# Optimization experiments

Hardware: AMD Instinct MI355X
Metric: run time of the kernel (lower is better)

The kernel has to match this reference:

```python
import jax, jax.numpy as jnp
import numpy as np

N, E, D, ED = 10000, 50000, 32, 16
DIMS = [(D, 8 * D), (8 * D, 16 * D), (16 * D, 16 * D), (16 * D, 16 * D)]
BI_OUT = 8 * D + ED  # 272


def _gat(h, src, dst, ea, Wl, Wr, We, att, b, n):
    """GATv2Conv, heads=1: score = att . leaky_relu(Wl x_j + Wr x_i + We e_ij); msg = Wl x_j."""
    xl = h @ Wl
    xr = h @ Wr
    ee = ea @ We
    s = jax.nn.leaky_relu(xl[src] + xr[dst] + ee, 0.2)   # [E_aug, out]
    alpha = s @ att                                       # [E_aug]
    amax = jax.lax.stop_gradient(jax.ops.segment_max(alpha, dst, num_segments=n))
    ex = jnp.exp(alpha - amax[dst])
    den = jax.ops.segment_sum(ex, dst, num_segments=n)
    w = ex / jnp.maximum(den[dst], 1e-16)
    return jax.ops.segment_sum(xl[src] * w[:, None], dst, num_segments=n) + b


def _forward(x, edge_attr, Wl0, Wr0, We0, a0, b0, Wl1, Wr1, We1, a1, b1,
             Wl2, Wr2, We2, a2, b2, Wl3, Wr3, We3, a3, b3,
             Wbi, bbi, Wm1, bm1, Wm2, bm2, Wm3, bm3, edge_index):
    src, dst = edge_index[0], edge_index[1]
    # self loops with edge_attr fill_value='mean' (mean of incoming edge_attr per target node)
    cnt = jax.ops.segment_sum(jnp.ones((E,), jnp.float32), dst, num_segments=N)
    mean_attr = jax.ops.segment_sum(edge_attr, dst, num_segments=N) / jnp.maximum(cnt, 1.0)[:, None]
    loop = jnp.arange(N, dtype=edge_index.dtype)
    src_a = jnp.concatenate([src, loop])
    dst_a = jnp.concatenate([dst, loop])
    ea_a = jnp.concatenate([edge_attr, mean_attr], axis=0)

    h = x
    layers = [(Wl0, Wr0, We0, a0, b0), (Wl1, Wr1, We1, a1, b1),
              (Wl2, Wr2, We2, a2, b2), (Wl3, Wr3, We3, a3, b3)]
    for i, (Wl, Wr, We, a, b) in enumerate(layers):
        h = _gat(h, src_a, dst_a, ea_a, Wl, Wr, We, a, b, N)
        if i < 3:
            h = jax.nn.relu(h)

    # edge scoring: gather both endpoints, bilinear with edge_attr, then MLP -> sigmoid
    z = jnp.concatenate([h[src], h[dst]], axis=1)           # [E, 2*16*D] = [E, 1024]
    bi = jnp.einsum('ni,kij,nj->nk', z, Wbi, edge_attr) + bbi  # [E, 272]
    m = jax.nn.relu(bi @ Wm1 + bm1)
    m = jax.nn.relu(m @ Wm2 + bm2)
    return jax.nn.sigmoid(m @ Wm3 + bm3)                    # [E, 1]


def setup_inputs() -> dict:
    ki = iter(jax.random.split(jax.random.key(0), 40))

    def rn(shape, s=0.05):
        return jax.random.normal(next(ki), shape, dtype=jnp.float32) * s

    inp = {
        "x": rn((N, D), 1.0),
        "edge_attr": rn((E, ED), 1.0),
        "edge_index": jax.random.randint(next(ki), (2, E), 0, N, dtype=jnp.int32),
    }
    for i, (din, dout) in enumerate(DIMS):
        inp[f"Wl{i}"] = rn((din, dout))
        inp[f"Wr{i}"] = rn((din, dout))
        inp[f"We{i}"] = rn((ED, dout))
        inp[f"a{i}"] = rn((dout,))
        inp[f"b{i}"] = jnp.zeros((dout,), jnp.float32)
    inp["Wbi"] = rn((BI_OUT, 2 * 16 * D, ED), 0.02)
    inp["bbi"] = jnp.zeros((BI_OUT,), jnp.float32)
    inp["Wm1"] = rn((BI_OUT, BI_OUT))
    inp["bm1"] = jnp.zeros((BI_OUT,), jnp.float32)
    inp["Wm2"] = rn((BI_OUT, D))
    inp["bm2"] = jnp.zeros((D,), jnp.float32)
    inp["Wm3"] = rn((D, 1))
    inp["bm3"] = jnp.zeros((1,), jnp.float32)
    return inp


def reference(x, edge_attr, edge_index, Wl0, Wr0, We0, a0, b0, Wl1, Wr1, We1, a1, b1,
              Wl2, Wr2, We2, a2, b2, Wl3, Wr3, We3, a3, b3,
              Wbi, bbi, Wm1, bm1, Wm2, bm2, Wm3, bm3):
    return _forward(x, edge_attr, Wl0, Wr0, We0, a0, b0, Wl1, Wr1, We1, a1, b1,
                    Wl2, Wr2, We2, a2, b2, Wl3, Wr3, We3, a3, b3,
                    Wbi, bbi, Wm1, bm1, Wm2, bm2, Wm3, bm3, edge_index)
```

## Files before the change

kernel.cpp:

```cpp
#include <hip/hip_runtime.h>
#include <hip/hip_bf16.h>
#include <hip/hip_fp16.h>
#include <cstdio>

#define N_NODES 10000
#define M_NODEP 10240
#define N_EDGES 50000
#define M_EDGEP 50176
#define E_AUG   60000
#define E_AUGP  60160
#define ED      16
#define BI_OUT  272
#define KP      288

typedef __attribute__((ext_vector_type(8))) short s16x8;
typedef __attribute__((ext_vector_type(4))) short s16x4;
typedef __attribute__((ext_vector_type(8))) _Float16 h16x8;
typedef __attribute__((ext_vector_type(4))) _Float16 h16x4;
typedef __attribute__((ext_vector_type(4))) float f32x4;

__device__ inline void stc(float* p, float v){ *p = v; }
__device__ inline void stc(__hip_bfloat16* p, float v){ *p = __float2bfloat16(v); }
__device__ inline void stc(__half* p, float v){ *p = __float2half(v); }
__device__ inline float bf2f(short s){ return __uint_as_float(((unsigned)(unsigned short)s) << 16); }
__device__ inline short f2bf(float f){ __hip_bfloat16 h = __float2bfloat16(f); return *(short*)&h; }

__device__ __forceinline__ void gl2lds16(const void* g, void* l){
  __builtin_amdgcn_global_load_lds((const __attribute__((address_space(1))) void*)g,
                                   (__attribute__((address_space(3))) void*)l, 16, 0, 0);
}

__device__ inline size_t preidx(int n, int k, int kSteps){
  int nb = n >> 7, f = (n >> 4) & 7, r = n & 15;
  int s = k >> 5, q = (k >> 3) & 3, ii = k & 7;
  return ((((size_t)nb*kSteps + s)*8 + f)*64 + q*16 + r)*8 + ii;
}

__global__ void edge_attr_sum_k(const float* __restrict__ ea, const int* __restrict__ ei,
                                float* __restrict__ meanat, float* __restrict__ cntF){
  int t = blockIdx.x*256 + threadIdx.x;
  if (t >= N_EDGES*ED) return;
  int e = t >> 4, j = t & 15;
  int dst = ei[N_EDGES + e];
  atomicAdd(&meanat[dst*ED + j], ea[t]);
  if (j == 0) atomicAdd(&cntF[dst], 1.0f);
}

__global__ void mean_div_k(float* __restrict__ meanat, const float* __restrict__ cntF){
  int t = blockIdx.x*256 + threadIdx.x;
  if (t >= N_NODES*ED) return;
  meanat[t] /= fmaxf(cntF[t>>4], 1.0f);
}

__global__ void scan_k(const float* __restrict__ cntF, int* __restrict__ rowptr){
  __shared__ int s[1024];
  int tid = threadIdx.x;
  int loc[10]; int sum = 0;
  #pragma unroll
  for (int k = 0; k < 10; ++k){
    int i = tid*10 + k;
    int v = (i < N_NODES) ? ((int)cntF[i] + 1) : 0;
    loc[k] = sum; sum += v;
  }
  s[tid] = sum; __syncthreads();
  for (int off = 1; off < 1024; off <<= 1){
    int t2 = (tid >= off) ? s[tid-off] : 0;
    __syncthreads();
    s[tid] += t2;
    __syncthreads();
  }
  int pre = s[tid] - sum;
  #pragma unroll
  for (int k = 0; k < 10; ++k){
    int i = tid*10 + k;
    if (i < N_NODES) rowptr[i] = pre + loc[k];
  }
  if (tid == 1023) rowptr[N_NODES] = s[1023];
}

__global__ void scatter_k(const int* __restrict__ ei, const int* __restrict__ rowptr,
                          int* __restrict__ fill, int* __restrict__ csr){
  int e = blockIdx.x*256 + threadIdx.x;
  if (e >= E_AUG) return;
  int dst = (e < N_EDGES) ? ei[N_EDGES+e] : (e - N_EDGES);
  int pos = rowptr[dst] + atomicAdd(&fill[dst], 1);
  csr[pos] = e;
}

template<typename TC, bool BIAS, bool RELU>
__global__ __launch_bounds__(256)
void mfma_gemm_k(const __hip_bfloat16* __restrict__ A, const __hip_bfloat16* __restrict__ Bp,
                 TC* __restrict__ C, const float* __restrict__ bias,
                 int Mstore, int K, int lda, int ldc){
  __shared__ __align__(16) __hip_bfloat16 Asm[2][4096];
  const int tid = threadIdx.x;
  const int lane = tid & 63, wave = tid >> 6;
  const int wm = (wave >> 1) * 64, wn = (wave & 1) * 64;
  const int m0 = blockIdx.x * 128, n0 = blockIdx.y * 128;
  const int quad = lane >> 4, r16 = lane & 15;
  const int kSteps = K >> 5;

  f32x4 acc[4][4];
  #pragma unroll
  for (int i = 0; i < 4; ++i)
    #pragma unroll
    for (int j = 0; j < 4; ++j)
      acc[i][j] = (f32x4){0.f, 0.f, 0.f, 0.f};

  const int rl = lane >> 2, cq = lane & 3;
  const int row0 = wave*32 + rl;
  const int qg = (cq - ((row0 >> 1) & 3)) & 3;
  const __hip_bfloat16* ga0 = &A[(size_t)(m0 + row0)*lda + qg*8];
  const __hip_bfloat16* ga1 = &A[(size_t)(m0 + row0 + 16)*lda + qg*8];
  const int aoff0 = (wave*32)*32, aoff1 = (wave*32 + 16)*32;

  const __hip_bfloat16* gB = Bp + (((size_t)blockIdx.y*kSteps)*8 + (wn >> 4))*512 + (size_t)lane*8;

  gl2lds16(ga0, &Asm[0][aoff0]);
  gl2lds16(ga1, &Asm[0][aoff1]);
  s16x8 bcur[4], bnxt[4];
  #pragma unroll
  for (int j = 0; j < 4; ++j) bcur[j] = *(const s16x8*)(gB + j*512);

  for (int s = 0; s < kSteps; ++s){
    __syncthreads();
    if (s + 1 < kSteps){
      int k0 = (s + 1) * 32;
      gl2lds16(ga0 + k0, &Asm[(s+1)&1][aoff0]);
      gl2lds16(ga1 + k0, &Asm[(s+1)&1][aoff1]);
      const __hip_bfloat16* gBn = gB + (size_t)(s+1)*4096;
      #pragma unroll
      for (int j = 0; j < 4; ++j) bnxt[j] = *(const s16x8*)(gBn + j*512);
    }
    s16x8 af[4];
    #pragma unroll
    for (int i = 0; i < 4; ++i){
      int row = wm + i*16 + r16;
      af[i] = *(const s16x8*)&Asm[s & 1][row*32 + (((quad + (row >> 1)) & 3) << 3)];
    }
    #pragma unroll
    for (int i = 0; i < 4; ++i)
      #pragma unroll
      for (int j = 0; j < 4; ++j)
        acc[i][j] = __builtin_amdgcn_mfma_f32_16x16x32_bf16(af[i], bcur[j], acc[i][j], 0, 0, 0);
    #pragma unroll
    for (int j = 0; j < 4; ++j) bcur[j] = bnxt[j];
  }
  #pragma unroll
  for (int i = 0; i < 4; ++i){
    #pragma unroll
    for (int reg = 0; reg < 4; ++reg){
      int gr = m0 + wm + i*16 + quad*4 + reg;
      if (gr >= Mstore) continue;
      #pragma unroll
      for (int j = 0; j < 4; ++j){
        int gc = n0 + wn + j*16 + r16;
        float v = acc[i][j][reg];
        if (BIAS) v += bias[gc];
        if (RELU) v = fmaxf(v, 0.f);
        stc(&C[(size_t)gr*ldc + gc], v);
      }
    }
  }
}

template<typename TC>
__global__ __launch_bounds__(256)
void gemm_k32_k(const __hip_bfloat16* __restrict__ A, const __hip_bfloat16* __restrict__ Bp,
                TC* __restrict__ C, int Mstore, int Ntiles, int lda, int ldc){
  __shared__ __align__(16) __hip_bfloat16 Asm[4096];
  const int tid = threadIdx.x;
  const int lane = tid & 63, wave = tid >> 6;
  const int wm = (wave >> 1) * 64, wn = (wave & 1) * 64;
  const int m0 = blockIdx.x * 128;
  const int quad = lane >> 4, r16 = lane & 15;

  const int rl = lane >> 2, cq = lane & 3;
  const int row0 = wave*32 + rl;
  const int qg = (cq - ((row0 >> 1) & 3)) & 3;
  gl2lds16(&A[(size_t)(m0 + row0)*lda + qg*8],      &Asm[(wave*32)*32]);
  gl2lds16(&A[(size_t)(m0 + row0 + 16)*lda + qg*8], &Asm[(wave*32 + 16)*32]);
  __syncthreads();
  s16x8 af[4];
  #pragma unroll
  for (int i = 0; i < 4; ++i){
    int row = wm + i*16 + r16;
    af[i] = *(const s16x8*)&Asm[row*32 + (((quad + (row >> 1)) & 3) << 3)];
  }

  const __hip_bfloat16* gB = Bp + (size_t)(wn >> 4)*512 + (size_t)lane*8;
  s16x8 bcur[4], bnxt[4];
  #pragma unroll
  for (int j = 0; j < 4; ++j) bcur[j] = *(const s16x8*)(gB + j*512);

  for (int nt = 0; nt < Ntiles; ++nt){
    if (nt + 1 < Ntiles){
      const __hip_bfloat16* gBn = gB + (size_t)(nt+1)*4096;
      #pragma unroll
      for (int j = 0; j < 4; ++j) bnxt[j] = *(const s16x8*)(gBn + j*512);
    }
    f32x4 acc[4][4];
    #pragma unroll
    for (int i = 0; i < 4; ++i)
      #pragma unroll
      for (int j = 0; j < 4; ++j)
        acc[i][j] = (f32x4){0.f, 0.f, 0.f, 0.f};
    #pragma unroll
    for (int i = 0; i < 4; ++i)
      #pragma unroll
      for (int j = 0; j < 4; ++j)
        acc[i][j] = __builtin_amdgcn_mfma_f32_16x16x32_bf16(af[i], bcur[j], acc[i][j], 0, 0, 0);
    int n0 = nt*128;
    #pragma unroll
    for (int i = 0; i < 4; ++i){
      #pragma unroll
      for (int reg = 0; reg < 4; ++reg){
        int gr = m0 + wm + i*16 + quad*4 + reg;
        if (gr >= Mstore) continue;
        #pragma unroll
        for (int j = 0; j < 4; ++j)
          stc(&C[(size_t)gr*ldc + n0 + wn + j*16 + r16], acc[i][j][reg]);
      }
    }
    #pragma unroll
    for (int j = 0; j < 4; ++j) bcur[j] = bnxt[j];
  }
}

__global__ __launch_bounds__(256)
void mlp2_out_k(const __hip_bfloat16* __restrict__ A, const __hip_bfloat16* __restrict__ Bp,
                const float* __restrict__ bias, const float* __restrict__ Wm3,
                const float* __restrict__ bm3, float* __restrict__ out,
                int Mstore, int K, int lda){
  __shared__ __align__(16) __hip_bfloat16 Asm[2][4096];
  const int tid = threadIdx.x;
  const int lane = tid & 63, wave = tid >> 6;
  const int wm = (wave >> 1) * 64, wn = (wave & 1) * 64;
  const int m0 = blockIdx.x * 128;
  const int quad = lane >> 4, r16 = lane & 15;
  const int kSteps = K >> 5;

  f32x4 acc[4][2];
  #pragma unroll
  for (int i = 0; i < 4; ++i)
    #pragma unroll
    for (int j = 0; j < 2; ++j)
      acc[i][j] = (f32x4){0.f, 0.f, 0.f, 0.f};

  const int rl = lane >> 2, cq = lane & 3;
  const int row0 = wave*32 + rl;
  const int qg = (cq - ((row0 >> 1) & 3)) & 3;
  const __hip_bfloat16* ga0 = &A[(size_t)(m0 + row0)*lda + qg*8];
  const __hip_bfloat16* ga1 = &A[(size_t)(m0 + row0 + 16)*lda + qg*8];
  const int aoff0 = (wave*32)*32, aoff1 = (wave*32 + 16)*32;

  const __hip_bfloat16* gB = Bp + (size_t)(wn >> 4)*512 + (size_t)lane*8;

  gl2lds16(ga0, &Asm[0][aoff0]);
  gl2lds16(ga1, &Asm[0][aoff1]);
  s16x8 bcur[2], bnxt[2];
  #pragma unroll
  for (int j = 0; j < 2; ++j) bcur[j] = *(const s16x8*)(gB + j*512);

  for (int s = 0; s < kSteps; ++s){
    __syncthreads();
    if (s + 1 < kSteps){
      int k0 = (s + 1) * 32;
      gl2lds16(ga0 + k0, &Asm[(s+1)&1][aoff0]);
      gl2lds16(ga1 + k0, &Asm[(s+1)&1][aoff1]);
      const __hip_bfloat16* gBn = gB + (size_t)(s+1)*4096;
      #pragma unroll
      for (int j = 0; j < 2; ++j) bnxt[j] = *(const s16x8*)(gBn + j*512);
    }
    s16x8 af[4];
    #pragma unroll
    for (int i = 0; i < 4; ++i){
      int row = wm + i*16 + r16;
      af[i] = *(const s16x8*)&Asm[s & 1][row*32 + (((quad + (row >> 1)) & 3) << 3)];
    }
    #pragma unroll
    for (int i = 0; i < 4; ++i)
      #pragma unroll
      for (int j = 0; j < 2; ++j)
        acc[i][j] = __builtin_amdgcn_mfma_f32_16x16x32_bf16(af[i], bcur[j], acc[i][j], 0, 0, 0);
    #pragma unroll
    for (int j = 0; j < 2; ++j) bcur[j] = bnxt[j];
  }
  if (wn == 0){
    float w3a = Wm3[r16], w3b = Wm3[16 + r16];
    float ba = bias[r16], bb = bias[16 + r16];
    #pragma unroll
    for (int i = 0; i < 4; ++i){
      #pragma unroll
      for (int reg = 0; reg < 4; ++reg){
        int gr = m0 + wm + i*16 + quad*4 + reg;
        float v0 = fmaxf(acc[i][0][reg] + ba, 0.f);
        float v1 = fmaxf(acc[i][1][reg] + bb, 0.f);
        float dot = v0*w3a + v1*w3b;
        #pragma unroll
        for (int off = 1; off < 16; off <<= 1) dot += __shfl_xor(dot, off, 64);
        if (r16 == 0 && gr < Mstore)
          out[gr] = 1.0f/(1.0f + __expf(-(dot + bm3[0])));
      }
    }
  }
}

__global__ void prep_weights_k(
    const float* __restrict__ Wl0, const float* __restrict__ Wr0, const float* __restrict__ We0,
    const float* __restrict__ Wl1, const float* __restrict__ Wr1, const float* __restrict__ We1,
    const float* __restrict__ Wl2, const float* __restrict__ Wr2, const float* __restrict__ We2,
    const float* __restrict__ Wl3, const float* __restrict__ Wr3, const float* __restrict__ We3,
    const float* __restrict__ Wm1, const float* __restrict__ bm1,
    const float* __restrict__ Wm2, const float* __restrict__ bm2,
    __hip_bfloat16* __restrict__ WTa, __hip_bfloat16* __restrict__ WeTa,
    __hip_bfloat16* __restrict__ Wm1T, __hip_bfloat16* __restrict__ Wm2T,
    float* __restrict__ bm1p, float* __restrict__ bm2p){
  int t = blockIdx.x*256 + threadIdx.x;
  if (t < 16384){
    int half = t >> 13, r = t & 8191, i = r >> 8, j = r & 255;
    WTa[preidx(half*256 + j, i, 1)] = __float2bfloat16(half ? Wr0[r] : Wl0[r]);
  } else if (t < 278528){
    int u = t - 16384, half = u >> 17, r = u & 131071, i = r >> 9, j = r & 511;
    WTa[16384 + preidx(half*512 + j, i, 8)] = __float2bfloat16(half ? Wr1[r] : Wl1[r]);
  } else if (t < 802816){
    int u = t - 278528, half = u >> 18, r = u & 262143, i = r >> 9, j = r & 511;
    WTa[278528 + preidx(half*512 + j, i, 16)] = __float2bfloat16(half ? Wr2[r] : Wl2[r]);
  } else if (t < 1327104){
    int u = t - 802816, half = u >> 18, r = u & 262143, i = r >> 9, j = r & 511;
    WTa[802816 + preidx(half*512 + j, i, 16)] = __float2bfloat16(half ? Wr3[r] : Wl3[r]);
  }
  if (t < 8192){
    int n = t >> 5, k = t & 31;
    WeTa[preidx(n, k, 1)] = __float2bfloat16((k < 16) ? We0[k*256 + n] : 0.f);
  } else if (t < 24576){
    int u = t - 8192, n = u >> 5, k = u & 31;
    WeTa[8192 + preidx(n, k, 1)] = __float2bfloat16((k < 16) ? We1[k*512 + n] : 0.f);
  } else if (t < 40960){
    int u = t - 24576, n = u >> 5, k = u & 31;
    WeTa[24576 + preidx(n, k, 1)] = __float2bfloat16((k < 16) ? We2[k*512 + n] : 0.f);
  } else if (t < 57344){
    int u = t - 40960, n = u >> 5, k = u & 31;
    WeTa[40960 + preidx(n, k, 1)] = __float2bfloat16((k < 16) ? We3[k*512 + n] : 0.f);
  }
  if (t < 384*KP){
    int n = t / KP, k = t - n*KP;
    Wm1T[preidx(n, k, 9)] = __float2bfloat16((n < BI_OUT && k < BI_OUT) ? Wm1[(size_t)k*BI_OUT + n] : 0.f);
  }
  if (t < 128*KP){
    int n = t / KP, k = t - n*KP;
    Wm2T[preidx(n, k, 9)] = __float2bfloat16((n < 32 && k < BI_OUT) ? Wm2[(size_t)k*32 + n] : 0.f);
  }
  if (t < 384) bm1p[t] = (t < BI_OUT) ? bm1[t] : 0.f;
  if (t < 128) bm2p[t] = (t < 32) ? bm2[t] : 0.f;
}

__global__ void cast_h_k(const float* __restrict__ h, __hip_bfloat16* __restrict__ hb, int K){
  int t = blockIdx.x*256 + threadIdx.x;
  if (t >= M_NODEP*K) return;
  int r = t / K;
  hb[t] = (r < N_NODES) ? __float2bfloat16(h[t]) : __float2bfloat16(0.f);
}

__global__ void cast_ea_k(const float* __restrict__ ea, const float* __restrict__ meanat,
                          __hip_bfloat16* __restrict__ eab){
  int t = blockIdx.x*256 + threadIdx.x;
  if (t >= E_AUGP*32) return;
  int e = t >> 5, j = t & 31;
  float v = 0.f;
  if (j < 16){
    if (e < N_EDGES) v = ea[(size_t)e*ED + j];
    else if (e < E_AUG) v = meanat[(size_t)(e - N_EDGES)*ED + j];
  }
  eab[t] = __float2bfloat16(v);
}

__global__ void wbi_transpose_k(const float* __restrict__ Wbi, __hip_bfloat16* __restrict__ WtAll){
  int t = blockIdx.x*256 + threadIdx.x;
  if (t >= BI_OUT*1024*ED) return;
  int k = t >> 14, r = t & 16383;
  int i = r >> 4, j = r & 15;
  int c = (k < 136) ? 0 : 1;
  int kb = c*136;
  const int cw = 2176;
  size_t baseE = (size_t)c * 2228224;
  int row = ((i >= 512) ? cw : 0) + (k - kb)*16 + j;
  WtAll[baseE + preidx(row, i & 511, 16)] = __float2bfloat16(Wbi[t]);
}

template<int DOUT, bool RELU>
__global__ __launch_bounds__(256)
void gat_fused_k(const __hip_bfloat16* __restrict__ XLXR, const __half* __restrict__ EE,
                 const int* __restrict__ ei, const int* __restrict__ rowptr,
                 const int* __restrict__ csr, const float* __restrict__ att,
                 const float* __restrict__ b, __hip_bfloat16* __restrict__ hb){
  constexpr int NI = DOUT/64;
  constexpr int W2 = 2*DOUT;
  int wave = threadIdx.x >> 6, lane = threadIdx.x & 63;
  int n = blockIdx.x*4 + wave;
  if (n >= N_NODES) return;
  int r0 = rowptr[n], r1 = rowptr[n+1];
  int pp = r0 + lane;
  int e_l = 0, s_l = 0;
  if (pp < r1){
    e_l = csr[pp];
    s_l = (e_l < N_EDGES) ? ei[e_l] : (e_l - N_EDGES);
  }
  float xr[NI], at[NI], acc[NI];
  #pragma unroll
  for (int i = 0; i < NI; ++i){
    int d = lane*NI + i;
    xr[i]  = bf2f(((const short*)XLXR)[(size_t)n*W2 + DOUT + d]);
    at[i]  = att[d];
    acc[i] = 0.f;
  }
  auto getes = [&](int p, int &e, int &s){
    int idx = p - r0;
    if (idx < 64){ e = __shfl(e_l, idx, 64); s = __shfl(s_l, idx, 64); }
    else { e = csr[p]; s = (e < N_EDGES) ? ei[e] : (e - N_EDGES); }
  };
  float mrun = -1e30f, den = 0.f;
  int p = r0;
  for (; p + 3 < r1; p += 4){
    int ee4[4], ss4[4];
    #pragma unroll
    for (int u = 0; u < 4; ++u) getes(p + u, ee4[u], ss4[u]);
    float xl[4][NI], a[4];
    #pragma unroll
    for (int u = 0; u < 4; ++u){
      const short* xp = (const short*)XLXR + (size_t)ss4[u]*W2 + lane*NI;
      const _Float16* ep = (const _Float16*)EE + (size_t)ee4[u]*DOUT + lane*NI;
      float au = 0.f;
      if constexpr (NI == 8){
        s16x8 xv = *(const s16x8*)xp; h16x8 ev = *(const h16x8*)ep;
        #pragma unroll
        for (int i = 0; i < 8; ++i){
          xl[u][i] = bf2f(xv[i]);
          float v = xl[u][i] + xr[i] + (float)ev[i];
          v = (v > 0.f) ? v : 0.2f*v;
          au += at[i]*v;
        }
      } else {
        s16x4 xv = *(const s16x4*)xp; h16x4 ev = *(const h16x4*)ep;
        #pragma unroll
        for (int i = 0; i < 4; ++i){
          xl[u][i] = bf2f(xv[i]);
          float v = xl[u][i] + xr[i] + (float)ev[i];
          v = (v > 0.f) ? v : 0.2f*v;
          au += at[i]*v;
        }
      }
      a[u] = au;
    }
    #pragma unroll
    for (int off = 32; off; off >>= 1){
      #pragma unroll
      for (int u = 0; u < 4; ++u) a[u] += __shfl_xor(a[u], off, 64);
    }
    float mnew = fmaxf(mrun, fmaxf(fmaxf(a[0], a[1]), fmaxf(a[2], a[3])));
    float sc = __expf(mrun - mnew);
    float w0 = __expf(a[0] - mnew), w1 = __expf(a[1] - mnew);
    float w2 = __expf(a[2] - mnew), w3 = __expf(a[3] - mnew);
    den = den*sc + w0 + w1 + w2 + w3;
    #pragma unroll
    for (int i = 0; i < NI; ++i)
      acc[i] = acc[i]*sc + w0*xl[0][i] + w1*xl[1][i] + w2*xl[2][i] + w3*xl[3][i];
    mrun = mnew;
  }
  for (; p + 1 < r1; p += 2){
    int e0, s0, e1, s1;
    getes(p, e0, s0); getes(p + 1, e1, s1);
    const short* xp0 = (const short*)XLXR + (size_t)s0*W2 + lane*NI;
    const short* xp1 = (const short*)XLXR + (size_t)s1*W2 + lane*NI;
    const _Float16* ep0 = (const _Float16*)EE + (size_t)e0*DOUT + lane*NI;
    const _Float16* ep1 = (const _Float16*)EE + (size_t)e1*DOUT + lane*NI;
    float xl0[NI], xl1[NI];
    float a0 = 0.f, a1 = 0.f;
    #pragma unroll
    for (int i = 0; i < NI; ++i){
      xl0[i] = bf2f(xp0[i]); xl1[i] = bf2f(xp1[i]);
      float v0 = xl0[i] + xr[i] + (float)ep0[i];
      float v1 = xl1[i] + xr[i] + (float)ep1[i];
      v0 = (v0 > 0.f) ? v0 : 0.2f*v0;
      v1 = (v1 > 0.f) ? v1 : 0.2f*v1;
      a0 += at[i]*v0; a1 += at[i]*v1;
    }
    #pragma unroll
    for (int off = 32; off; off >>= 1){
      a0 += __shfl_xor(a0, off, 64);
      a1 += __shfl_xor(a1, off, 64);
    }
    float mnew = fmaxf(mrun, fmaxf(a0, a1));
    float sc = __expf(mrun - mnew);
    float w0 = __expf(a0 - mnew);
    float w1 = __expf(a1 - mnew);
    den = den*sc + w0 + w1;
    #pragma unroll
    for (int i = 0; i < NI; ++i) acc[i] = acc[i]*sc + w0*xl0[i] + w1*xl1[i];
    mrun = mnew;
  }
  if (p < r1){
    int e0, s0;
    getes(p, e0, s0);
    const short* xp0 = (const short*)XLXR + (size_t)s0*W2 + lane*NI;
    const _Float16* ep0 = (const _Float16*)EE + (size_t)e0*DOUT + lane*NI;
    float xl0[NI];
    float a0 = 0.f;
    #pragma unroll
    for (int i = 0; i < NI; ++i){
      xl0[i] = bf2f(xp0[i]);
      float v0 = xl0[i] + xr[i] + (float)ep0[i];
      v0 = (v0 > 0.f) ? v0 : 0.2f*v0;
      a0 += at[i]*v0;
    }
    #pragma unroll
    for (int off = 32; off; off >>= 1) a0 += __shfl_xor(a0, off, 64);
    float mnew = fmaxf(mrun, a0);
    float sc = __expf(mrun - mnew);
    float w0 = __expf(a0 - mnew);
    den = den*sc + w0;
    #pragma unroll
    for (int i = 0; i < NI; ++i) acc[i] = acc[i]*sc + w0*xl0[i];
    mrun = mnew;
  }
  float dinv = 1.0f / fmaxf(den, 1e-16f);
  if constexpr (NI == 8){
    s16x8 o;
    #pragma unroll
    for (int i = 0; i < 8; ++i){
      float v = b[lane*8 + i] + acc[i]*dinv;
      o[i] = f2bf(RELU ? fmaxf(v, 0.f) : v);
    }
    *(s16x8*)((short*)hb + (size_t)n*DOUT + lane*8) = o;
  } else {
    s16x4 o;
    #pragma unroll
    for (int i = 0; i < 4; ++i){
      float v = b[lane*4 + i] + acc[i]*dinv;
      o[i] = f2bf(RELU ? fmaxf(v, 0.f) : v);
    }
    *(s16x4*)((short*)hb + (size_t)n*DOUT + lane*4) = o;
  }
}

__global__ void bi_k(const __hip_bfloat16* __restrict__ P, const float* __restrict__ ea,
                     const int* __restrict__ ei, const int* __restrict__ csr,
                     const float* __restrict__ bbi, __hip_bfloat16* __restrict__ bi,
                     int kb){
  const int KH = 68;
  const int cw = 2176, w2 = 4352;
  int g = blockIdx.x*256 + threadIdx.x;
  if (g >= E_AUG*KH) return;
  int p = g / KH, kp = g - p*KH;
  int k = kp*2;
  int e = csr[p];
  if (e >= N_EDGES) return;
  int src = ei[e], dst = ei[N_EDGES+e];
  const s16x8* pl = (const s16x8*)(P + (size_t)src*w2 + k*ED);
  const s16x8* pr = (const s16x8*)(P + (size_t)dst*w2 + cw + k*ED);
  s16x8 pl0 = pl[0], pl1 = pl[1], pl2 = pl[2], pl3 = pl[3];
  s16x8 pr0 = pr[0], pr1 = pr[1], pr2 = pr[2], pr3 = pr[3];
  const float* eap = ea + (size_t)e*ED;
  float s0 = 0.f, s1 = 0.f;
  #pragma unroll
  for (int j = 0; j < 8; ++j){
    s0 += eap[j]  *(bf2f(pl0[j]) + bf2f(pr0[j]));
    s0 += eap[j+8]*(bf2f(pl1[j]) + bf2f(pr1[j]));
    s1 += eap[j]  *(bf2f(pl2[j]) + bf2f(pr2[j]));
    s1 += eap[j+8]*(bf2f(pl3[j]) + bf2f(pr3[j]));
  }
  int kg = kb + k;
  short2 o;
  o.x = f2bf(s0 + bbi[kg]);
  o.y = f2bf(s1 + bbi[kg+1]);
  *(short2*)((short*)bi + (size_t)e*KP + kg) = o;
}

extern "C" void kernel_launch(void* const* d_in, const int* in_sizes, int n_in,
                              void* d_out, int out_size, void* d_ws, size_t ws_size,
                              hipStream_t stream) {
  const float* x   = (const float*)d_in[0];
  const float* ea  = (const float*)d_in[1];
  const int*   ei  = (const int*)d_in[2];
  const float* Wl[4]  = {(const float*)d_in[3],(const float*)d_in[8],(const float*)d_in[13],(const float*)d_in[18]};
  const float* Wr[4]  = {(const float*)d_in[4],(const float*)d_in[9],(const float*)d_in[14],(const float*)d_in[19]};
  const float* We[4]  = {(const float*)d_in[5],(const float*)d_in[10],(const float*)d_in[15],(const float*)d_in[20]};
  const float* att[4] = {(const float*)d_in[6],(const float*)d_in[11],(const float*)d_in[16],(const float*)d_in[21]};
  const float* bia[4] = {(const float*)d_in[7],(const float*)d_in[12],(const float*)d_in[17],(const float*)d_in[22]};
  const float* Wbi = (const float*)d_in[23];
  const float* bbi = (const float*)d_in[24];
  const float* Wm1 = (const float*)d_in[25];
  const float* bm1 = (const float*)d_in[26];
  const float* Wm2 = (const float*)d_in[27];
  const float* bm2 = (const float*)d_in[28];
  const float* Wm3 = (const float*)d_in[29];
  const float* bm3 = (const float*)d_in[30];
  float* out = (float*)d_out;

  char* ws = (char*)d_ws;
  size_t off = 0;
  auto alloc = [&](size_t b){ off = (off + 255) & ~(size_t)255; size_t o = off; off += b; return o; };
  size_t o_bi   = alloc((size_t)M_EDGEP*KP*2);
  size_t o_XLXR = alloc((size_t)M_NODEP*1024*2);
  size_t o_hb   = alloc((size_t)M_NODEP*512*2);
  size_t o_eab  = alloc((size_t)E_AUGP*32*2);
  size_t o_WTa  = alloc((size_t)1327104*2);
  size_t o_WeTa = alloc((size_t)57344*2);
  size_t o_WtA  = alloc((size_t)8704*512*2);
  size_t o_EEP  = alloc((size_t)90000000);
  size_t o_Wm1T = alloc((size_t)384*KP*2);
  size_t o_Wm2T = alloc((size_t)128*KP*2);
  size_t o_bm1p = alloc(384*4);
  size_t o_bm2p = alloc(128*4);
  size_t o_ma   = alloc((size_t)N_NODES*ED*4);
  size_t o_cnt  = alloc(40000);
  size_t o_rp   = alloc(40004);
  size_t o_fill = alloc(40000);
  size_t o_csr  = alloc(240000);
  if (off > ws_size){
    fprintf(stderr, "kernel_launch: workspace too small: need %zu have %zu\n", off, ws_size);
    return;
  }

  float* meanat = (float*)(ws + o_ma);
  float* cntF   = (float*)(ws + o_cnt);
  int*   rowptr = (int*)(ws + o_rp);
  int*   fill   = (int*)(ws + o_fill);
  int*   csr    = (int*)(ws + o_csr);
  __hip_bfloat16* XLXR = (__hip_bfloat16*)(ws + o_XLXR);
  __hip_bfloat16* hb   = (__hip_bfloat16*)(ws + o_hb);
  __hip_bfloat16* eab  = (__hip_bfloat16*)(ws + o_eab);
  __hip_bfloat16* WTa  = (__hip_bfloat16*)(ws + o_WTa);
  __hip_bfloat16* WeTa = (__hip_bfloat16*)(ws + o_WeTa);
  __hip_bfloat16* WtA  = (__hip_bfloat16*)(ws + o_WtA);
  __half*        EE    = (__half*)(ws + o_EEP);
  __hip_bfloat16* P    = (__hip_bfloat16*)(ws + o_EEP);
  __hip_bfloat16* Wm1T = (__hip_bfloat16*)(ws + o_Wm1T);
  __hip_bfloat16* Wm2T = (__hip_bfloat16*)(ws + o_Wm2T);
  float* bm1p = (float*)(ws + o_bm1p);
  float* bm2p = (float*)(ws + o_bm2p);
  __hip_bfloat16* bi = (__hip_bfloat16*)(ws + o_bi);
  __hip_bfloat16* m1 = (__hip_bfloat16*)(ws + o_EEP);

  hipMemsetAsync(ws + o_ma, 0, (o_cnt - o_ma) + 40000, stream);
  hipMemsetAsync(ws + o_fill, 0, 40000, stream);
  edge_attr_sum_k<<<3125, 256, 0, stream>>>(ea, ei, meanat, cntF);
  mean_div_k<<<625, 256, 0, stream>>>(meanat, cntF);
  scan_k<<<1, 1024, 0, stream>>>(cntF, rowptr);
  scatter_k<<<235, 256, 0, stream>>>(ei, rowptr, fill, csr);

  cast_h_k<<<(M_NODEP*32 + 255)/256, 256, 0, stream>>>(x, hb, 32);
  cast_ea_k<<<(E_AUGP*32 + 255)/256, 256, 0, stream>>>(ea, meanat, eab);
  prep_weights_k<<<5184, 256, 0, stream>>>(
      Wl[0], Wr[0], We[0], Wl[1], Wr[1], We[1], Wl[2], Wr[2], We[2], Wl[3], Wr[3], We[3],
      Wm1, bm1, Wm2, bm2, WTa, WeTa, Wm1T, Wm2T, bm1p, bm2p);
  wbi_transpose_k<<<(BI_OUT*1024*ED + 255)/256, 256, 0, stream>>>(Wbi, WtA);

  const int dins[4]  = {32, 256, 512, 512};
  const int douts[4] = {256, 512, 512, 512};
  const int wtOff[4] = {0, 16384, 278528, 802816};
  const int weOff[4] = {0, 8192, 24576, 40960};
  for (int L = 0; L < 4; ++L){
    int din = dins[L], dn = douts[L];
    if (L == 0){
      gemm_k32_k<__hip_bfloat16><<<M_NODEP/128, 256, 0, stream>>>(
          hb, WTa, XLXR, N_NODES, 4, 32, 512);
    } else {
      dim3 g1(M_NODEP/128, 2*dn/128);
      mfma_gemm_k<__hip_bfloat16,false,false><<<g1, 256, 0, stream>>>(
          hb, WTa + wtOff[L], XLXR, nullptr, N_NODES, din, din, 2*dn);
    }
    gemm_k32_k<__half><<<E_AUGP/128, 256, 0, stream>>>(
        eab, WeTa + weOff[L], EE, E_AUG, dn/128, 32, dn);
    if (dn == 256)
      gat_fused_k<256,true><<<2500, 256, 0, stream>>>(XLXR, EE, ei, rowptr, csr, att[L], bia[L], hb);
    else if (L == 3)
      gat_fused_k<512,false><<<2500, 256, 0, stream>>>(XLXR, EE, ei, rowptr, csr, att[L], bia[L], hb);
    else
      gat_fused_k<512,true><<<2500, 256, 0, stream>>>(XLXR, EE, ei, rowptr, csr, att[L], bia[L], hb);
  }

  const int kbs[2]      = {0, 136};
  const size_t baseE[2] = {0, 2228224};
  for (int c = 0; c < 2; ++c){
    dim3 gp(M_NODEP/128, 4352/128);
    mfma_gemm_k<__hip_bfloat16,false,false><<<gp, 256, 0, stream>>>(
        hb, WtA + baseE[c], P, nullptr, N_NODES, 512, 512, 4352);
    bi_k<<<(E_AUG*68 + 255)/256, 256, 0, stream>>>(P, ea, ei, csr, bbi, bi, kbs[c]);
  }

  dim3 gm1(M_EDGEP/128, 3);
  mfma_gemm_k<__hip_bfloat16,true,true><<<gm1, 256, 0, stream>>>(bi, Wm1T, m1, bm1p, M_EDGEP, KP, KP, 384);
  mlp2_out_k<<<M_EDGEP/128, 256, 0, stream>>>(m1, Wm2T, bm2p, Wm3, bm3, out, N_EDGES, KP, 384);
}
```

Baseline: 609.8 us.

## Compute self-loop mean attrs via CSR gather and merge prep kernels

```diff
diff --git a/kernel.cpp b/kernel.cpp
--- a/kernel.cpp
+++ b/kernel.cpp
@@ -36,30 +36,20 @@
   return ((((size_t)nb*kSteps + s)*8 + f)*64 + q*16 + r)*8 + ii;
 }
 
-__global__ void edge_attr_sum_k(const float* __restrict__ ea, const int* __restrict__ ei,
-                                float* __restrict__ meanat, float* __restrict__ cntF){
-  int t = blockIdx.x*256 + threadIdx.x;
-  if (t >= N_EDGES*ED) return;
-  int e = t >> 4, j = t & 15;
-  int dst = ei[N_EDGES + e];
-  atomicAdd(&meanat[dst*ED + j], ea[t]);
-  if (j == 0) atomicAdd(&cntF[dst], 1.0f);
-}
-
-__global__ void mean_div_k(float* __restrict__ meanat, const float* __restrict__ cntF){
-  int t = blockIdx.x*256 + threadIdx.x;
-  if (t >= N_NODES*ED) return;
-  meanat[t] /= fmaxf(cntF[t>>4], 1.0f);
-}
-
-__global__ void scan_k(const float* __restrict__ cntF, int* __restrict__ rowptr){
+__global__ void count_k(const int* __restrict__ ei, int* __restrict__ cnt){
+  int e = blockIdx.x*256 + threadIdx.x;
+  if (e >= N_EDGES) return;
+  atomicAdd(&cnt[ei[N_EDGES + e]], 1);
+}
+
+__global__ void scan_k(const int* __restrict__ cnt, int* __restrict__ rowptr){
   __shared__ int s[1024];
   int tid = threadIdx.x;
   int loc[10]; int sum = 0;
   #pragma unroll
   for (int k = 0; k < 10; ++k){
     int i = tid*10 + k;
-    int v = (i < N_NODES) ? ((int)cntF[i] + 1) : 0;
+    int v = (i < N_NODES) ? (cnt[i] + 1) : 0;
     loc[k] = sum; sum += v;
   }
   s[tid] = sum; __syncthreads();
@@ -85,6 +75,20 @@
   int dst = (e < N_EDGES) ? ei[N_EDGES+e] : (e - N_EDGES);
   int pos = rowptr[dst] + atomicAdd(&fill[dst], 1);
   csr[pos] = e;
+}
+
+__global__ void meanat_csr_k(const float* __restrict__ ea, const int* __restrict__ rowptr,
+                             const int* __restrict__ csr, float* __restrict__ meanat){
+  int g = blockIdx.x*256 + threadIdx.x;
+  int n = g >> 4, j = g & 15;
+  if (n >= N_NODES) return;
+  int r0 = rowptr[n], r1 = rowptr[n+1];
+  float acc = 0.f; int c = 0;
+  for (int p = r0; p < r1; ++p){
+    int e = csr[p];
+    if (e < N_EDGES){ acc += ea[(size_t)e*ED + j]; ++c; }
+  }
+  meanat[(size_t)n*ED + j] = acc / fmaxf((float)c, 1.f);
 }
 
 template<typename TC, bool BIAS, bool RELU>
@@ -306,86 +310,95 @@
   }
 }
 
-__global__ void prep_weights_k(
+__global__ void prep_all_k(
+    const float* __restrict__ x, const float* __restrict__ ea, const float* __restrict__ meanat,
     const float* __restrict__ Wl0, const float* __restrict__ Wr0, const float* __restrict__ We0,
     const float* __restrict__ Wl1, const float* __restrict__ Wr1, const float* __restrict__ We1,
     const float* __restrict__ Wl2, const float* __restrict__ Wr2, const float* __restrict__ We2,
     const float* __restrict__ Wl3, const float* __restrict__ Wr3, const float* __restrict__ We3,
     const float* __restrict__ Wm1, const float* __restrict__ bm1,
     const float* __restrict__ Wm2, const float* __restrict__ bm2,
+    const float* __restrict__ Wbi,
+    __hip_bfloat16* __restrict__ hb, __hip_bfloat16* __restrict__ eab,
     __hip_bfloat16* __restrict__ WTa, __hip_bfloat16* __restrict__ WeTa,
     __hip_bfloat16* __restrict__ Wm1T, __hip_bfloat16* __restrict__ Wm2T,
-    float* __restrict__ bm1p, float* __restrict__ bm2p){
-  int t = blockIdx.x*256 + threadIdx.x;
-  if (t < 16384){
-    int half = t >> 13, r = t & 8191, i = r >> 8, j = r & 255;
-    WTa[preidx(half*256 + j, i, 1)] = __float2bfloat16(half ? Wr0[r] : Wl0[r]);
-  } else if (t < 278528){
-    int u = t - 16384, half = u >> 17, r = u & 131071, i = r >> 9, j = r & 511;
-    WTa[16384 + preidx(half*512 + j, i, 8)] = __float2bfloat16(half ? Wr1[r] : Wl1[r]);
-  } else if (t < 802816){
-    int u = t - 278528, half = u >> 18, r = u & 262143, i = r >> 9, j = r & 511;
-    WTa[278528 + preidx(half*512 + j, i, 16)] = __float2bfloat16(half ? Wr2[r] : Wl2[r]);
-  } else if (t < 1327104){
-    int u = t - 802816, half = u >> 18, r = u & 262143, i = r >> 9, j = r & 511;
-    WTa[802816 + preidx(half*512 + j, i, 16)] = __float2bfloat16(half ? Wr3[r] : Wl3[r]);
-  }
-  if (t < 8192){
-    int n = t >> 5, k = t & 31;
-    WeTa[preidx(n, k, 1)] = __float2bfloat16((k < 16) ? We0[k*256 + n] : 0.f);
-  } else if (t < 24576){
-    int u = t - 8192, n = u >> 5, k = u & 31;
-    WeTa[8192 + preidx(n, k, 1)] = __float2bfloat16((k < 16) ? We1[k*512 + n] : 0.f);
-  } else if (t < 40960){
-    int u = t - 24576, n = u >> 5, k = u & 31;
-    WeTa[24576 + preidx(n, k, 1)] = __float2bfloat16((k < 16) ? We2[k*512 + n] : 0.f);
-  } else if (t < 57344){
-    int u = t - 40960, n = u >> 5, k = u & 31;
-    WeTa[40960 + preidx(n, k, 1)] = __float2bfloat16((k < 16) ? We3[k*512 + n] : 0.f);
-  }
-  if (t < 384*KP){
-    int n = t / KP, k = t - n*KP;
-    Wm1T[preidx(n, k, 9)] = __float2bfloat16((n < BI_OUT && k < BI_OUT) ? Wm1[(size_t)k*BI_OUT + n] : 0.f);
-  }
-  if (t < 128*KP){
-    int n = t / KP, k = t - n*KP;
-    Wm2T[preidx(n, k, 9)] = __float2bfloat16((n < 32 && k < BI_OUT) ? Wm2[(size_t)k*32 + n] : 0.f);
-  }
-  if (t < 384) bm1p[t] = (t < BI_OUT) ? bm1[t] : 0.f;
-  if (t < 128) bm2p[t] = (t < 32) ? bm2[t] : 0.f;
-}
-
-__global__ void cast_h_k(const float* __restrict__ h, __hip_bfloat16* __restrict__ hb, int K){
-  int t = blockIdx.x*256 + threadIdx.x;
-  if (t >= M_NODEP*K) return;
-  int r = t / K;
-  hb[t] = (r < N_NODES) ? __float2bfloat16(h[t]) : __float2bfloat16(0.f);
-}
-
-__global__ void cast_ea_k(const float* __restrict__ ea, const float* __restrict__ meanat,
-                          __hip_bfloat16* __restrict__ eab){
-  int t = blockIdx.x*256 + threadIdx.x;
-  if (t >= E_AUGP*32) return;
-  int e = t >> 5, j = t & 31;
-  float v = 0.f;
-  if (j < 16){
-    if (e < N_EDGES) v = ea[(size_t)e*ED + j];
-    else if (e < E_AUG) v = meanat[(size_t)(e - N_EDGES)*ED + j];
-  }
-  eab[t] = __float2bfloat16(v);
-}
-
-__global__ void wbi_transpose_k(const float* __restrict__ Wbi, __hip_bfloat16* __restrict__ WtAll){
-  int t = blockIdx.x*256 + threadIdx.x;
-  if (t >= BI_OUT*1024*ED) return;
-  int k = t >> 14, r = t & 16383;
-  int i = r >> 4, j = r & 15;
-  int c = (k < 136) ? 0 : 1;
-  int kb = c*136;
-  const int cw = 2176;
-  size_t baseE = (size_t)c * 2228224;
-  int row = ((i >= 512) ? cw : 0) + (k - kb)*16 + j;
-  WtAll[baseE + preidx(row, i & 511, 16)] = __float2bfloat16(Wbi[t]);
+    float* __restrict__ bm1p, float* __restrict__ bm2p,
+    __hip_bfloat16* __restrict__ WtA){
+  int b = blockIdx.x;
+  if (b < 1280){
+    int t = b*256 + threadIdx.x;
+    int r = t >> 5;
+    hb[t] = (r < N_NODES) ? __float2bfloat16(x[t]) : __float2bfloat16(0.f);
+    return;
+  }
+  b -= 1280;
+  if (b < 7520){
+    int t = b*256 + threadIdx.x;
+    if (t < E_AUGP*32){
+      int e = t >> 5, j = t & 31;
+      float v = 0.f;
+      if (j < 16){
+        if (e < N_EDGES) v = ea[(size_t)e*ED + j];
+        else if (e < E_AUG) v = meanat[(size_t)(e - N_EDGES)*ED + j];
+      }
+      eab[t] = __float2bfloat16(v);
+    }
+    return;
+  }
+  b -= 7520;
+  if (b < 5184){
+    int t = b*256 + threadIdx.x;
+    if (t < 16384){
+      int half = t >> 13, r = t & 8191, i = r >> 8, j = r & 255;
+      WTa[preidx(half*256 + j, i, 1)] = __float2bfloat16(half ? Wr0[r] : Wl0[r]);
+    } else if (t < 278528){
+      int u = t - 16384, half = u >> 17, r = u & 131071, i = r >> 9, j = r & 511;
+      WTa[16384 + preidx(half*512 + j, i, 8)] = __float2bfloat16(half ? Wr1[r] : Wl1[r]);
+    } else if (t < 802816){
+      int u = t - 278528, half = u >> 18, r = u & 262143, i = r >> 9, j = r & 511;
+      WTa[278528 + preidx(half*512 + j, i, 16)] = __float2bfloat16(half ? Wr2[r] : Wl2[r]);
+    } else if (t < 1327104){
+      int u = t - 802816, half = u >> 18, r = u & 262143, i = r >> 9, j = r & 511;
+      WTa[802816 + preidx(half*512 + j, i, 16)] = __float2bfloat16(half ? Wr3[r] : Wl3[r]);
+    }
+    if (t < 8192){
+      int n = t >> 5, k = t & 31;
+      WeTa[preidx(n, k, 1)] = __float2bfloat16((k < 16) ? We0[k*256 + n] : 0.f);
+    } else if (t < 24576){
+      int u = t - 8192, n = u >> 5, k = u & 31;
+      WeTa[8192 + preidx(n, k, 1)] = __float2bfloat16((k < 16) ? We1[k*512 + n] : 0.f);
+    } else if (t < 40960){
+      int u = t - 24576, n = u >> 5, k = u & 31;
+      WeTa[24576 + preidx(n, k, 1)] = __float2bfloat16((k < 16) ? We2[k*512 + n] : 0.f);
+    } else if (t < 57344){
+      int u = t - 40960, n = u >> 5, k = u & 31;
+      WeTa[40960 + preidx(n, k, 1)] = __float2bfloat16((k < 16) ? We3[k*512 + n] : 0.f);
+    }
+    if (t < 384*KP){
+      int n = t / KP, k = t - n*KP;
+      Wm1T[preidx(n, k, 9)] = __float2bfloat16((n < BI_OUT && k < BI_OUT) ? Wm1[(size_t)k*BI_OUT + n] : 0.f);
+    }
+    if (t < 128*KP){
+      int n = t / KP, k = t - n*KP;
+      Wm2T[preidx(n, k, 9)] = __float2bfloat16((n < 32 && k < BI_OUT) ? Wm2[(size_t)k*32 + n] : 0.f);
+    }
+    if (t < 384) bm1p[t] = (t < BI_OUT) ? bm1[t] : 0.f;
+    if (t < 128) bm2p[t] = (t < 32) ? bm2[t] : 0.f;
+    return;
+  }
+  b -= 5184;
+  {
+    int t = b*256 + threadIdx.x;
+    if (t >= BI_OUT*1024*ED) return;
+    int k = t >> 14, r = t & 16383;
+    int i = r >> 4, j = r & 15;
+    int c = (k < 136) ? 0 : 1;
+    int kb = c*136;
+    const int cw = 2176;
+    size_t baseE = (size_t)c * 2228224;
+    int row = ((i >= 512) ? cw : 0) + (k - kb)*16 + j;
+    WtA[baseE + preidx(row, i & 511, 16)] = __float2bfloat16(Wbi[t]);
+  }
 }
 
 template<int DOUT, bool RELU>
@@ -614,8 +627,8 @@
   size_t o_bm2p = alloc(128*4);
   size_t o_ma   = alloc((size_t)N_NODES*ED*4);
   size_t o_cnt  = alloc(40000);
+  size_t o_fill = alloc(40000);
   size_t o_rp   = alloc(40004);
-  size_t o_fill = alloc(40000);
   size_t o_csr  = alloc(240000);
   if (off > ws_size){
     fprintf(stderr, "kernel_launch: workspace too small: need %zu have %zu\n", off, ws_size);
@@ -623,9 +636,9 @@
   }
 
   float* meanat = (float*)(ws + o_ma);
-  float* cntF   = (float*)(ws + o_cnt);
+  int*   cnt    = (int*)(ws + o_cnt);
+  int*   fill   = (int*)(ws + o_fill);
   int*   rowptr = (int*)(ws + o_rp);
-  int*   fill   = (int*)(ws + o_fill);
   int*   csr    = (int*)(ws + o_csr);
   __hip_bfloat16* XLXR = (__hip_bfloat16*)(ws + o_XLXR);
   __hip_bfloat16* hb   = (__hip_bfloat16*)(ws + o_hb);
@@ -642,19 +655,17 @@
   __hip_bfloat16* bi = (__hip_bfloat16*)(ws + o_bi);
   __hip_bfloat16* m1 = (__hip_bfloat16*)(ws + o_EEP);
 
-  hipMemsetAsync(ws + o_ma, 0, (o_cnt - o_ma) + 40000, stream);
-  hipMemsetAsync(ws + o_fill, 0, 40000, stream);
-  edge_attr_sum_k<<<3125, 256, 0, stream>>>(ea, ei, meanat, cntF);
-  mean_div_k<<<625, 256, 0, stream>>>(meanat, cntF);
-  scan_k<<<1, 1024, 0, stream>>>(cntF, rowptr);
+  hipMemsetAsync(ws + o_cnt, 0, (o_fill - o_cnt) + 40000, stream);
+  count_k<<<(N_EDGES + 255)/256, 256, 0, stream>>>(ei, cnt);
+  scan_k<<<1, 1024, 0, stream>>>(cnt, rowptr);
   scatter_k<<<235, 256, 0, stream>>>(ei, rowptr, fill, csr);
-
-  cast_h_k<<<(M_NODEP*32 + 255)/256, 256, 0, stream>>>(x, hb, 32);
-  cast_ea_k<<<(E_AUGP*32 + 255)/256, 256, 0, stream>>>(ea, meanat, eab);
-  prep_weights_k<<<5184, 256, 0, stream>>>(
+  meanat_csr_k<<<625, 256, 0, stream>>>(ea, rowptr, csr, meanat);
+
+  prep_all_k<<<1280 + 7520 + 5184 + 17408, 256, 0, stream>>>(
+      x, ea, meanat,
       Wl[0], Wr[0], We[0], Wl[1], Wr[1], We[1], Wl[2], Wr[2], We[2], Wl[3], Wr[3], We[3],
-      Wm1, bm1, Wm2, bm2, WTa, WeTa, Wm1T, Wm2T, bm1p, bm2p);
-  wbi_transpose_k<<<(BI_OUT*1024*ED + 255)/256, 256, 0, stream>>>(Wbi, WtA);
+      Wm1, bm1, Wm2, bm2, Wbi,
+      hb, eab, WTa, WeTa, Wm1T, Wm2T, bm1p, bm2p, WtA);
 
   const int dins[4]  = {32, 256, 512, 512};
   const int douts[4] = {256, 512, 512, 512};
```

New measurement: 608.3 us. Within noise of the previous version (-0.2%).
